# Performance work log

Measured on AMD Instinct MI355X. Metric: run time of the kernel, lower is better.

## Reference

```python
import jax, jax.numpy as jnp
import numpy as np

B, T, I, H, O = 4096, 200, 2, 64, 2


def setup_inputs() -> dict:
    key = jax.random.key(0)
    ks = jax.random.split(key, 7)
    s = 1.0 / np.sqrt(H)  # PyTorch LSTM init scale
    return {
        "x": jax.random.normal(ks[0], (B, T, I), dtype=jnp.float32),
        "W_ih": jax.random.uniform(ks[1], (4 * H, I), jnp.float32, -s, s),
        "W_hh": jax.random.uniform(ks[2], (4 * H, H), jnp.float32, -s, s),
        "b_ih": jax.random.uniform(ks[3], (4 * H,), jnp.float32, -s, s),
        "b_hh": jax.random.uniform(ks[4], (4 * H,), jnp.float32, -s, s),
        "W_fc": jax.random.uniform(ks[5], (O, H), jnp.float32, -s, s),
        "b_fc": jax.random.uniform(ks[6], (O,), jnp.float32, -s, s),
    }


def reference(x, W_ih, W_hh, b_ih, b_hh, W_fc, b_fc):
    # Precompute input-to-gate projections for all timesteps in one GEMM.
    # xg: [T, B, 4H] (time-major for scan)
    xg = jnp.einsum("bti,gi->tbg", x, W_ih) + (b_ih + b_hh)

    def step(carry, xt):
        h, c = carry  # [B, H] each
        gates = xt + h @ W_hh.T  # [B, 4H]
        i_g, f_g, g_g, o_g = jnp.split(gates, 4, axis=-1)  # PyTorch order: i, f, g, o
        i = jax.nn.sigmoid(i_g)
        f = jax.nn.sigmoid(f_g)
        g = jnp.tanh(g_g)
        o = jax.nn.sigmoid(o_g)
        c = f * c + i * g
        h = o * jnp.tanh(c)
        return (h, c), None

    h0 = jnp.zeros((x.shape[0], W_hh.shape[1]), dtype=x.dtype)
    c0 = jnp.zeros_like(h0)
    (h_last, _), _ = jax.lax.scan(step, (h0, c0), xg)
    return h_last @ W_fc.T + b_fc  # [B, O]
```

## Files before the change

kernel.cpp:

```cpp
#include <hip/hip_runtime.h>
#include <hip/hip_bf16.h>


#define B_ 4096
#define T_ 200
#define H_ 64

typedef _Float16 half8 __attribute__((ext_vector_type(8)));
typedef float f32x4 __attribute__((ext_vector_type(4)));

__device__ __forceinline__ float fsig(float x) {
    return __builtin_amdgcn_rcpf(1.0f + __builtin_amdgcn_exp2f(-1.4426950408889634f * x));
}
__device__ __forceinline__ float ftanh(float x) {
    return 1.0f - 2.0f * __builtin_amdgcn_rcpf(1.0f + __builtin_amdgcn_exp2f(2.8853900817779268f * x));
}

__global__ __launch_bounds__(512) void lstm_kernel(
    const float* __restrict__ x,
    const float* __restrict__ W_ih,
    const float* __restrict__ W_hh,
    const float* __restrict__ b_ih,
    const float* __restrict__ b_hh,
    const float* __restrict__ W_fc,
    const float* __restrict__ b_fc,
    float* __restrict__ out)
{
    __shared__ float xs[16][400];
    __shared__ _Float16 h16[2][16][72];
    __shared__ float hf[16][65];
    __shared__ float wfc[130];

    const int tid  = threadIdx.x;
    const int lane = tid & 63;
    const int w    = tid >> 6;
    const int wq   = w & 3;
    const int half = w >> 2;
    const int cidx = lane & 15;
    const int grp  = lane >> 4;
    const int r0   = blockIdx.x * 16;

    for (int i4 = tid; i4 < 1600; i4 += 512) {
        const int row = i4 / 100;
        const int j4  = i4 - row * 100;
        const float4 v = reinterpret_cast<const float4*>(x + (size_t)(r0 + row) * 400)[j4];
        reinterpret_cast<float4*>(&xs[row][0])[j4] = v;
    }
    for (int i = tid; i < 2 * 16 * 72 / 2; i += 512)
        reinterpret_cast<unsigned int*>(&h16[0][0][0])[i] = 0u;
    if (tid < 130) wfc[tid] = (tid < 128) ? W_fc[tid] : b_fc[tid - 128];

    half8 bfrag[4][2];
    float wi0[4], wi1[4], bs[4];
    const int u = wq * 16 + cidx;
    #pragma unroll
    for (int m = 0; m < 4; ++m) {
        const int g = m * 64 + u;
        wi0[m] = W_ih[g * 2 + 0];
        wi1[m] = W_ih[g * 2 + 1];
        bs[m]  = b_ih[g] + b_hh[g];
        #pragma unroll
        for (int kt = 0; kt < 2; ++kt) {
            const float* p = W_hh + g * 64 + kt * 32 + grp * 8;
            const float4 lo = reinterpret_cast<const float4*>(p)[0];
            const float4 hi = reinterpret_cast<const float4*>(p)[1];
            half8 f;
            f[0] = (_Float16)lo.x; f[1] = (_Float16)lo.y;
            f[2] = (_Float16)lo.z; f[3] = (_Float16)lo.w;
            f[4] = (_Float16)hi.x; f[5] = (_Float16)hi.y;
            f[6] = (_Float16)hi.z; f[7] = (_Float16)hi.w;
            bfrag[m][kt] = f;
        }
    }

    float cst[2] = {0.f, 0.f};

    __syncthreads();

    for (int t = 0; t < T_; ++t) {
        const int rd = t & 1, wr = rd ^ 1;
        const half8 a0 = *reinterpret_cast<const half8*>(&h16[rd][cidx][grp * 8]);
        const half8 a1 = *reinterpret_cast<const half8*>(&h16[rd][cidx][32 + grp * 8]);

        f32x4 acc[4];
        #pragma unroll
        for (int m = 0; m < 4; ++m) {
            f32x4 a = {0.f, 0.f, 0.f, 0.f};
            a = __builtin_amdgcn_mfma_f32_16x16x32_f16(a0, bfrag[m][0], a, 0, 0, 0);
            a = __builtin_amdgcn_mfma_f32_16x16x32_f16(a1, bfrag[m][1], a, 0, 0, 0);
            acc[m] = a;
        }

        #pragma unroll
        for (int s = 0; s < 2; ++s) {
            const int r   = 2 * half + s;
            const int row = grp * 4 + r;
            const float2 xv = *reinterpret_cast<const float2*>(&xs[row][2 * t]);
            const float ip = acc[0][r] + fmaf(xv.y, wi1[0], fmaf(xv.x, wi0[0], bs[0]));
            const float fp = acc[1][r] + fmaf(xv.y, wi1[1], fmaf(xv.x, wi0[1], bs[1]));
            const float gp = acc[2][r] + fmaf(xv.y, wi1[2], fmaf(xv.x, wi0[2], bs[2]));
            const float op = acc[3][r] + fmaf(xv.y, wi1[3], fmaf(xv.x, wi0[3], bs[3]));
            const float ig = fsig(ip);
            const float fg = fsig(fp);
            const float gg = ftanh(gp);
            const float og = fsig(op);
            const float cv = fmaf(fg, cst[s], ig * gg);
            cst[s] = cv;
            const float hv = og * ftanh(cv);
            h16[wr][row][u] = (_Float16)hv;
            if (t == T_ - 1) hf[row][u] = hv;
        }
        __syncthreads();
    }

    if (tid < 32) {
        const int r = tid & 15;
        const int o = tid >> 4;
        float s = wfc[128 + o];
        #pragma unroll
        for (int k = 0; k < 64; ++k)
            s = fmaf(wfc[o * 64 + k], hf[r][k], s);
        out[(size_t)(r0 + r) * 2 + o] = s;
    }
}

extern "C" void kernel_launch(void* const* d_in, const int* in_sizes, int n_in,
                              void* d_out, int out_size, void* d_ws, size_t ws_size,
                              hipStream_t stream) {
    const float* x    = (const float*)d_in[0];
    const float* W_ih = (const float*)d_in[1];
    const float* W_hh = (const float*)d_in[2];
    const float* b_ih = (const float*)d_in[3];
    const float* b_hh = (const float*)d_in[4];
    const float* W_fc = (const float*)d_in[5];
    const float* b_fc = (const float*)d_in[6];
    float* out = (float*)d_out;

    lstm_kernel<<<B_ / 16, 512, 0, stream>>>(x, W_ih, W_hh, b_ih, b_hh, W_fc, b_fc, out);
}
```

Baseline: 129.5 us.

## Use 1024 threads with row-rotated MFMA so each lane handles one output row

The block grows from 8 to 16 waves. Each wave group rotates the A-operand rows (arow = cidx+qr), so the single accumulator element a[0] gives the needed row. Each thread then does the gate math for one (row, unit) pair instead of two, which halves per-thread activation work but doubles the MFMA work across the block. The bias is folded into the MFMA accumulator init, the fp32 final-h buffer is dropped in favour of reading the fp16 h for the FC (a small precision loss), and the xs row padding changes.

```diff
diff --git a/kernel.cpp b/kernel.cpp
--- a/kernel.cpp
+++ b/kernel.cpp
@@ -4,7 +4,6 @@
 
 #define B_ 4096
 #define T_ 200
-#define H_ 64
 
 typedef _Float16 half8 __attribute__((ext_vector_type(8)));
 typedef float f32x4 __attribute__((ext_vector_type(4)));
@@ -13,10 +12,10 @@
     return __builtin_amdgcn_rcpf(1.0f + __builtin_amdgcn_exp2f(-1.4426950408889634f * x));
 }
 __device__ __forceinline__ float ftanh(float x) {
-    return 1.0f - 2.0f * __builtin_amdgcn_rcpf(1.0f + __builtin_amdgcn_exp2f(2.8853900817779268f * x));
+    return fmaf(-2.0f, __builtin_amdgcn_rcpf(1.0f + __builtin_amdgcn_exp2f(2.8853900817779268f * x)), 1.0f);
 }
 
-__global__ __launch_bounds__(512) void lstm_kernel(
+__global__ __launch_bounds__(1024) void lstm_kernel(
     const float* __restrict__ x,
     const float* __restrict__ W_ih,
     const float* __restrict__ W_hh,
@@ -26,27 +25,26 @@
     const float* __restrict__ b_fc,
     float* __restrict__ out)
 {
-    __shared__ float xs[16][400];
+    __shared__ float xs[16][404];
     __shared__ _Float16 h16[2][16][72];
-    __shared__ float hf[16][65];
     __shared__ float wfc[130];
 
     const int tid  = threadIdx.x;
     const int lane = tid & 63;
     const int w    = tid >> 6;
     const int wq   = w & 3;
-    const int half = w >> 2;
+    const int qr   = w >> 2;
     const int cidx = lane & 15;
     const int grp  = lane >> 4;
     const int r0   = blockIdx.x * 16;
 
-    for (int i4 = tid; i4 < 1600; i4 += 512) {
+    for (int i4 = tid; i4 < 1600; i4 += 1024) {
         const int row = i4 / 100;
         const int j4  = i4 - row * 100;
-        const float4 v = reinterpret_cast<const float4*>(x + (size_t)(r0 + row) * 400)[j4];
-        reinterpret_cast<float4*>(&xs[row][0])[j4] = v;
+        reinterpret_cast<float4*>(&xs[row][0])[j4] =
+            reinterpret_cast<const float4*>(x + (size_t)(r0 + row) * 400)[j4];
     }
-    for (int i = tid; i < 2 * 16 * 72 / 2; i += 512)
+    for (int i = tid; i < 1152; i += 1024)
         reinterpret_cast<unsigned int*>(&h16[0][0][0])[i] = 0u;
     if (tid < 130) wfc[tid] = (tid < 128) ? W_fc[tid] : b_fc[tid - 128];
 
@@ -73,43 +71,35 @@
         }
     }
 
-    float cst[2] = {0.f, 0.f};
+    const int arow = (cidx + qr) & 15;
+    const int row  = (grp * 4 + qr) & 15;
+    float cst = 0.f;
 
     __syncthreads();
 
     for (int t = 0; t < T_; ++t) {
-        const int rd = t & 1, wr = rd ^ 1;
-        const half8 a0 = *reinterpret_cast<const half8*>(&h16[rd][cidx][grp * 8]);
-        const half8 a1 = *reinterpret_cast<const half8*>(&h16[rd][cidx][32 + grp * 8]);
+        const int rd = t & 1;
+        const _Float16* hb = &h16[rd][0][0];
+        const half8 a0 = *reinterpret_cast<const half8*>(hb + arow * 72 + grp * 8);
+        const half8 a1 = *reinterpret_cast<const half8*>(hb + arow * 72 + 32 + grp * 8);
+        const float2 xv = *reinterpret_cast<const float2*>(&xs[row][2 * t]);
 
-        f32x4 acc[4];
+        float pre[4];
         #pragma unroll
         for (int m = 0; m < 4; ++m) {
-            f32x4 a = {0.f, 0.f, 0.f, 0.f};
+            f32x4 a = {bs[m], bs[m], bs[m], bs[m]};
             a = __builtin_amdgcn_mfma_f32_16x16x32_f16(a0, bfrag[m][0], a, 0, 0, 0);
             a = __builtin_amdgcn_mfma_f32_16x16x32_f16(a1, bfrag[m][1], a, 0, 0, 0);
-            acc[m] = a;
+            pre[m] = fmaf(xv.y, wi1[m], fmaf(xv.x, wi0[m], a[0]));
         }
 
-        #pragma unroll
-        for (int s = 0; s < 2; ++s) {
-            const int r   = 2 * half + s;
-            const int row = grp * 4 + r;
-            const float2 xv = *reinterpret_cast<const float2*>(&xs[row][2 * t]);
-            const float ip = acc[0][r] + fmaf(xv.y, wi1[0], fmaf(xv.x, wi0[0], bs[0]));
-            const float fp = acc[1][r] + fmaf(xv.y, wi1[1], fmaf(xv.x, wi0[1], bs[1]));
-            const float gp = acc[2][r] + fmaf(xv.y, wi1[2], fmaf(xv.x, wi0[2], bs[2]));
-            const float op = acc[3][r] + fmaf(xv.y, wi1[3], fmaf(xv.x, wi0[3], bs[3]));
-            const float ig = fsig(ip);
-            const float fg = fsig(fp);
-            const float gg = ftanh(gp);
-            const float og = fsig(op);
-            const float cv = fmaf(fg, cst[s], ig * gg);
-            cst[s] = cv;
-            const float hv = og * ftanh(cv);
-            h16[wr][row][u] = (_Float16)hv;
-            if (t == T_ - 1) hf[row][u] = hv;
-        }
+        const float ig = fsig(pre[0]);
+        const float fg = fsig(pre[1]);
+        const float gg = ftanh(pre[2]);
+        const float og = fsig(pre[3]);
+        cst = fmaf(fg, cst, ig * gg);
+        const float hv = og * ftanh(cst);
+        h16[rd ^ 1][row][u] = (_Float16)hv;
         __syncthreads();
     }
 
@@ -119,7 +109,7 @@
         float s = wfc[128 + o];
         #pragma unroll
         for (int k = 0; k < 64; ++k)
-            s = fmaf(wfc[o * 64 + k], hf[r][k], s);
+            s = fmaf(wfc[o * 64 + k], (float)h16[0][r][k], s);
         out[(size_t)(r0 + r) * 2 + o] = s;
     }
 }
@@ -136,5 +126,5 @@
     const float* b_fc = (const float*)d_in[6];
     float* out = (float*)d_out;
 
-    lstm_kernel<<<B_ / 16, 512, 0, stream>>>(x, W_ih, W_hh, b_ih, b_hh, W_fc, b_fc, out);
+    lstm_kernel<<<B_ / 16, 1024, 0, stream>>>(x, W_ih, W_hh, b_ih, b_hh, W_fc, b_fc, out);
 }
```

Result: faster. 115.5 us (-10.8%).
